# Performance work log

Hardware: AMD Instinct MI355X
Metric: run time of the kernel (lower is better)

## Reference

```python
import jax, jax.numpy as jnp
import numpy as np

N, IN_DIM, OUT_DIM = 8192, 256, 64
NEG_BIG = -9e15
LRELU_SLOPE = 0.01  # torch F.leaky_relu default


def setup_inputs() -> dict:
    key = jax.random.key(0)
    k1, k2, k3, k4 = jax.random.split(key, 4)
    inp = jax.random.normal(k1, (N, IN_DIM), dtype=jnp.float32)
    adj = jax.random.randint(k2, (N, N), 0, 2, dtype=jnp.int32)
    # xavier_uniform with gain=1.414
    limW = 1.414 * np.sqrt(6.0 / (IN_DIM + OUT_DIM))
    W = jax.random.uniform(k3, (IN_DIM, OUT_DIM), minval=-limW, maxval=limW, dtype=jnp.float32)
    lima = 1.414 * np.sqrt(6.0 / (2 * OUT_DIM + 1))
    a = jax.random.uniform(k4, (2 * OUT_DIM, 1), minval=-lima, maxval=lima, dtype=jnp.float32)
    return {"input": inp, "adj": adj, "W": W, "a": a}


def reference(input, adj, W, a):
    h = input @ W                      # [N, D]
    a1, a2 = a[:OUT_DIM, 0], a[OUT_DIM:, 0]
    # e[i,j] = leaky_relu(a1.h_i + a2.h_j) == the concat-based score, no NxNx2D tensor
    f1 = h @ a1                        # [N]
    f2 = h @ a2                        # [N]
    e = jax.nn.leaky_relu(f1[:, None] + f2[None, :], negative_slope=LRELU_SLOPE)  # [N, N]
    face_Rhand = e[1, 2]
    face_Lhand = e[1, 3]
    Rhand_Lhand = e[3, 2]
    attention = jnp.where(adj > 0, e, jnp.float32(NEG_BIG))
    alpha = jax.nn.softmax(attention, axis=1)
    h_prime = alpha @ h                # [N, D]
    return (h_prime, face_Rhand, face_Lhand, Rhand_Lhand)
```

## Files before the change

kernel.cpp:

```cpp
#include <hip/hip_runtime.h>
#include <hip/hip_bf16.h>

#define GN 8192
#define KD 256
#define OD 64
#define LOG2E 1.44269504f
#define ASTR 260
#define NCH 16

typedef __attribute__((ext_vector_type(8))) short bf16x8;
typedef __attribute__((ext_vector_type(4))) float f32x4;

__device__ __forceinline__ float fexp2(float x) {
#if __has_builtin(__builtin_amdgcn_exp2f)
  return __builtin_amdgcn_exp2f(x);
#else
  return exp2f(x);
#endif
}

__device__ __forceinline__ void async_cp16(const void* g, void* l) {
  __builtin_amdgcn_global_load_lds(
      (const __attribute__((address_space(1))) unsigned int*)g,
      (__attribute__((address_space(3))) unsigned int*)l, 16, 0, 0);
}

__global__ __launch_bounds__(256) void gat_k1(
    const float* __restrict__ input, const float* __restrict__ W,
    const float* __restrict__ a, __hip_bfloat16* __restrict__ hT,
    float* __restrict__ f1p, float* __restrict__ f2p, float* __restrict__ out)
{
  __shared__ float Wl[KD * OD];
  __shared__ float inT[KD * 33];
  __shared__ float red1[8][32];
  __shared__ float red2[8][32];
  __shared__ float s1row[32];
  __shared__ float s2row[32];

  const int tid = threadIdx.x;
  const int i0 = blockIdx.x * 32;

  for (int idx = tid; idx < KD * OD / 4; idx += 256)
    ((float4*)Wl)[idx] = ((const float4*)W)[idx];

#pragma unroll
  for (int it = 0; it < 8; ++it) {
    int idx = tid + it * 256;
    int r = idx >> 6, k4 = idx & 63;
    float4 v = *(const float4*)(input + (long)(i0 + r) * KD + k4 * 4);
    inT[(k4 * 4 + 0) * 33 + r] = v.x;
    inT[(k4 * 4 + 1) * 33 + r] = v.y;
    inT[(k4 * 4 + 2) * 33 + r] = v.z;
    inT[(k4 * 4 + 3) * 33 + r] = v.w;
  }
  __syncthreads();

  const int r = tid & 31;
  const int cg = tid >> 5;
  float acc[8];
#pragma unroll
  for (int c = 0; c < 8; ++c) acc[c] = 0.f;

#pragma unroll 4
  for (int k = 0; k < KD; ++k) {
    float inv = inT[k * 33 + r];
    float4 wa = *(const float4*)&Wl[k * 64 + cg * 8];
    float4 wb = *(const float4*)&Wl[k * 64 + cg * 8 + 4];
    acc[0] += inv * wa.x; acc[1] += inv * wa.y;
    acc[2] += inv * wa.z; acc[3] += inv * wa.w;
    acc[4] += inv * wb.x; acc[5] += inv * wb.y;
    acc[6] += inv * wb.z; acc[7] += inv * wb.w;
  }

#pragma unroll
  for (int c = 0; c < 8; ++c)
    hT[(long)(cg * 8 + c) * GN + i0 + r] = __float2bfloat16(acc[c]);

  float s1 = 0.f, s2 = 0.f;
#pragma unroll
  for (int c = 0; c < 8; ++c) {
    s1 += acc[c] * a[cg * 8 + c];
    s2 += acc[c] * a[OD + cg * 8 + c];
  }
  red1[cg][r] = s1; red2[cg][r] = s2;
  __syncthreads();
  if (tid < 32) {
    float f1 = 0.f, f2 = 0.f;
#pragma unroll
    for (int g = 0; g < 8; ++g) { f1 += red1[g][tid]; f2 += red2[g][tid]; }
    s1row[tid] = f1; s2row[tid] = f2;
    f1p[i0 + tid] = f1 * LOG2E;
    f2p[i0 + tid] = f2 * LOG2E;
  }
  __syncthreads();
  if (blockIdx.x == 0 && tid == 0) {
    float e12 = s1row[1] + s2row[2];
    float e13 = s1row[1] + s2row[3];
    float e32 = s1row[3] + s2row[2];
    out[(long)GN * OD + 0] = fmaxf(e12, 0.01f * e12);
    out[(long)GN * OD + 1] = fmaxf(e13, 0.01f * e13);
    out[(long)GN * OD + 2] = fmaxf(e32, 0.01f * e32);
  }
}

__global__ __launch_bounds__(256, 4) void gat_k2(
    const int* __restrict__ adj, const __hip_bfloat16* __restrict__ hT,
    const float* __restrict__ f1p, const float* __restrict__ f2p,
    float* __restrict__ pn, float* __restrict__ pd)
{
  __shared__ int smem[2 * 16 * ASTR];
  float* pb = (float*)smem;
  float* sb = pb + 4 * 16 * 68;

  const int tid = threadIdx.x;
  const int lane = tid & 63;
  const int wv = tid >> 6;
  const int tn = lane & 15;
  const int quad = lane >> 4;
  const int rg = blockIdx.x >> 1;
  const int js = blockIdx.x & 1;
  const int i0 = rg * 16;
  const int jbase = js * 4096;

  const float f1r = f1p[i0 + tn];
  const int jo0 = (2 * wv) * 32 + quad * 8;
  const int jo1 = jo0 + 32;
  const __hip_bfloat16* hbase = hT + (long)tn * GN + jbase;
  const float* fpb = f2p + jbase;

  const int srow = wv * 4;
  const int* g0 = adj + (long)(i0 + srow + 0) * GN + jbase + lane * 4;
  const int* g1 = adj + (long)(i0 + srow + 1) * GN + jbase + lane * 4;
  const int* g2 = adj + (long)(i0 + srow + 2) * GN + jbase + lane * 4;
  const int* g3 = adj + (long)(i0 + srow + 3) * GN + jbase + lane * 4;

  f32x4 acc[4];
#pragma unroll
  for (int nf = 0; nf < 4; ++nf) acc[nf] = (f32x4){0.f, 0.f, 0.f, 0.f};
  f32x4 accS = (f32x4){0.f, 0.f, 0.f, 0.f};

  bf16x8 ones;
  {
    short ov = (tn == 0) ? (short)0x3F80 : (short)0;
#pragma unroll
    for (int i = 0; i < 8; ++i) ones[i] = ov;
  }

  async_cp16(g0, &smem[(srow + 0) * ASTR]);
  async_cp16(g1, &smem[(srow + 1) * ASTR]);
  async_cp16(g2, &smem[(srow + 2) * ASTR]);
  async_cp16(g3, &smem[(srow + 3) * ASTR]);
  bf16x8 B0[4], B1[4];
#pragma unroll
  for (int nf = 0; nf < 4; ++nf) {
    B0[nf] = *(const bf16x8*)(hbase + (long)nf * (16 * GN) + jo0);
    B1[nf] = *(const bf16x8*)(hbase + (long)nf * (16 * GN) + jo1);
  }
  __syncthreads();

  for (int c = 0; c < NCH; ++c) {
    const int cur = (c & 1) * (16 * ASTR);
    const int nxt = ((c & 1) ^ 1) * (16 * ASTR);
    if (c + 1 < NCH) {
      async_cp16(g0 + (c + 1) * 256, &smem[nxt + (srow + 0) * ASTR]);
      async_cp16(g1 + (c + 1) * 256, &smem[nxt + (srow + 1) * ASTR]);
      async_cp16(g2 + (c + 1) * 256, &smem[nxt + (srow + 2) * ASTR]);
      async_cp16(g3 + (c + 1) * 256, &smem[nxt + (srow + 3) * ASTR]);
    }

    const float4 f20 = *(const float4*)(fpb + c * 256 + jo0);
    const float4 f21 = *(const float4*)(fpb + c * 256 + jo0 + 4);
    const float4 f22 = *(const float4*)(fpb + c * 256 + jo1);
    const float4 f23 = *(const float4*)(fpb + c * 256 + jo1 + 4);
    const int4 a0 = *(const int4*)&smem[cur + tn * ASTR + jo0];
    const int4 a1 = *(const int4*)&smem[cur + tn * ASTR + jo0 + 4];
    const int4 a2 = *(const int4*)&smem[cur + tn * ASTR + jo1];
    const int4 a3 = *(const int4*)&smem[cur + tn * ASTR + jo1 + 4];

    union { bf16x8 v; unsigned u[4]; } w0, w1;
    {
      float e0 = f1r + f20.x, e1 = f1r + f20.y, e2 = f1r + f20.z, e3 = f1r + f20.w;
      float e4 = f1r + f21.x, e5 = f1r + f21.y, e6 = f1r + f21.z, e7 = f1r + f21.w;
      float v0 = fexp2((a0.x > 0) ? fmaxf(e0, 0.01f * e0) : -256.f);
      float v1 = fexp2((a0.y > 0) ? fmaxf(e1, 0.01f * e1) : -256.f);
      float v2 = fexp2((a0.z > 0) ? fmaxf(e2, 0.01f * e2) : -256.f);
      float v3 = fexp2((a0.w > 0) ? fmaxf(e3, 0.01f * e3) : -256.f);
      float v4 = fexp2((a1.x > 0) ? fmaxf(e4, 0.01f * e4) : -256.f);
      float v5 = fexp2((a1.y > 0) ? fmaxf(e5, 0.01f * e5) : -256.f);
      float v6 = fexp2((a1.z > 0) ? fmaxf(e6, 0.01f * e6) : -256.f);
      float v7 = fexp2((a1.w > 0) ? fmaxf(e7, 0.01f * e7) : -256.f);
      w0.u[0] = __builtin_amdgcn_perm(__float_as_uint(v1), __float_as_uint(v0), 0x07060302u);
      w0.u[1] = __builtin_amdgcn_perm(__float_as_uint(v3), __float_as_uint(v2), 0x07060302u);
      w0.u[2] = __builtin_amdgcn_perm(__float_as_uint(v5), __float_as_uint(v4), 0x07060302u);
      w0.u[3] = __builtin_amdgcn_perm(__float_as_uint(v7), __float_as_uint(v6), 0x07060302u);
    }
    {
      float e0 = f1r + f22.x, e1 = f1r + f22.y, e2 = f1r + f22.z, e3 = f1r + f22.w;
      float e4 = f1r + f23.x, e5 = f1r + f23.y, e6 = f1r + f23.z, e7 = f1r + f23.w;
      float v0 = fexp2((a2.x > 0) ? fmaxf(e0, 0.01f * e0) : -256.f);
      float v1 = fexp2((a2.y > 0) ? fmaxf(e1, 0.01f * e1) : -256.f);
      float v2 = fexp2((a2.z > 0) ? fmaxf(e2, 0.01f * e2) : -256.f);
      float v3 = fexp2((a2.w > 0) ? fmaxf(e3, 0.01f * e3) : -256.f);
      float v4 = fexp2((a3.x > 0) ? fmaxf(e4, 0.01f * e4) : -256.f);
      float v5 = fexp2((a3.y > 0) ? fmaxf(e5, 0.01f * e5) : -256.f);
      float v6 = fexp2((a3.z > 0) ? fmaxf(e6, 0.01f * e6) : -256.f);
      float v7 = fexp2((a3.w > 0) ? fmaxf(e7, 0.01f * e7) : -256.f);
      w1.u[0] = __builtin_amdgcn_perm(__float_as_uint(v1), __float_as_uint(v0), 0x07060302u);
      w1.u[1] = __builtin_amdgcn_perm(__float_as_uint(v3), __float_as_uint(v2), 0x07060302u);
      w1.u[2] = __builtin_amdgcn_perm(__float_as_uint(v5), __float_as_uint(v4), 0x07060302u);
      w1.u[3] = __builtin_amdgcn_perm(__float_as_uint(v7), __float_as_uint(v6), 0x07060302u);
    }

#pragma unroll
    for (int nf = 0; nf < 4; ++nf)
      acc[nf] = __builtin_amdgcn_mfma_f32_16x16x32_bf16(w0.v, B0[nf], acc[nf], 0, 0, 0);
    accS = __builtin_amdgcn_mfma_f32_16x16x32_bf16(w0.v, ones, accS, 0, 0, 0);
#pragma unroll
    for (int nf = 0; nf < 4; ++nf)
      acc[nf] = __builtin_amdgcn_mfma_f32_16x16x32_bf16(w1.v, B1[nf], acc[nf], 0, 0, 0);
    accS = __builtin_amdgcn_mfma_f32_16x16x32_bf16(w1.v, ones, accS, 0, 0, 0);

    if (c + 1 < NCH) {
#pragma unroll
      for (int nf = 0; nf < 4; ++nf) {
        B0[nf] = *(const bf16x8*)(hbase + (long)nf * (16 * GN) + (c + 1) * 256 + jo0);
        B1[nf] = *(const bf16x8*)(hbase + (long)nf * (16 * GN) + (c + 1) * 256 + jo1);
      }
    }
    __syncthreads();
  }

#pragma unroll
  for (int nf = 0; nf < 4; ++nf)
#pragma unroll
    for (int rgi = 0; rgi < 4; ++rgi)
      pb[(wv * 16 + quad * 4 + rgi) * 68 + nf * 16 + tn] = acc[nf][rgi];
  if (tn == 0) {
#pragma unroll
    for (int rgi = 0; rgi < 4; ++rgi)
      sb[wv * 16 + quad * 4 + rgi] = accS[rgi];
  }
  __syncthreads();
  for (int t = tid; t < 16 * OD; t += 256) {
    int rr = t >> 6, cc = t & 63;
    float num = pb[(0 * 16 + rr) * 68 + cc] + pb[(1 * 16 + rr) * 68 + cc] +
                pb[(2 * 16 + rr) * 68 + cc] + pb[(3 * 16 + rr) * 68 + cc];
    pn[((long)js * GN + i0 + rr) * OD + cc] = num;
  }
  if (tid < 16) {
    float den = sb[0 * 16 + tid] + sb[1 * 16 + tid] + sb[2 * 16 + tid] + sb[3 * 16 + tid];
    pd[(long)js * GN + i0 + tid] = den;
  }
}

__global__ __launch_bounds__(256) void gat_k3(
    const float* __restrict__ pn, const float* __restrict__ pd,
    float* __restrict__ out)
{
  long t = (long)blockIdx.x * 256 + threadIdx.x;
  int i = (int)(t >> 6);
  float num = pn[t] + pn[(long)GN * OD + t];
  float den = pd[i] + pd[GN + i];
  out[t] = num / den;
}

extern "C" void kernel_launch(void* const* d_in, const int* in_sizes, int n_in,
                              void* d_out, int out_size, void* d_ws, size_t ws_size,
                              hipStream_t stream) {
  const float* input = (const float*)d_in[0];
  const int* adj     = (const int*)d_in[1];
  const float* W     = (const float*)d_in[2];
  const float* a     = (const float*)d_in[3];
  float* out = (float*)d_out;

  char* ws = (char*)d_ws;
  __hip_bfloat16* hT = (__hip_bfloat16*)ws;
  float* f1p = (float*)(ws + (size_t)OD * GN * 2);
  float* f2p = f1p + GN;
  float* pn  = f2p + GN;
  float* pd  = pn + (size_t)2 * GN * OD;

  gat_k1<<<256, 256, 0, stream>>>(input, W, a, hT, f1p, f2p, out);
  gat_k2<<<1024, 256, 0, stream>>>(adj, hT, f1p, f2p, pn, pd);
  gat_k3<<<GN * OD / 256, 256, 0, stream>>>(pn, pd, out);
}
```

Before: 400.8 us.

## Tile h layout per 32 rows, stage f2 in LDS, register-staged adj prefetch

```diff
diff --git a/kernel.cpp b/kernel.cpp
--- a/kernel.cpp
+++ b/kernel.cpp
@@ -19,15 +19,9 @@
 #endif
 }
 
-__device__ __forceinline__ void async_cp16(const void* g, void* l) {
-  __builtin_amdgcn_global_load_lds(
-      (const __attribute__((address_space(1))) unsigned int*)g,
-      (__attribute__((address_space(3))) unsigned int*)l, 16, 0, 0);
-}
-
 __global__ __launch_bounds__(256) void gat_k1(
     const float* __restrict__ input, const float* __restrict__ W,
-    const float* __restrict__ a, __hip_bfloat16* __restrict__ hT,
+    const float* __restrict__ a, __hip_bfloat16* __restrict__ hTt,
     float* __restrict__ f1p, float* __restrict__ f2p, float* __restrict__ out)
 {
   __shared__ float Wl[KD * OD];
@@ -74,7 +68,8 @@
 
 #pragma unroll
   for (int c = 0; c < 8; ++c)
-    hT[(long)(cg * 8 + c) * GN + i0 + r] = __float2bfloat16(acc[c]);
+    hTt[(long)blockIdx.x * (OD * 32) + (cg * 8 + c) * 32 + r] =
+        __float2bfloat16(acc[c]);
 
   float s1 = 0.f, s2 = 0.f;
 #pragma unroll
@@ -103,13 +98,14 @@
   }
 }
 
-__global__ __launch_bounds__(256, 4) void gat_k2(
-    const int* __restrict__ adj, const __hip_bfloat16* __restrict__ hT,
+__global__ __launch_bounds__(256, 3) void gat_k2(
+    const int* __restrict__ adj, const __hip_bfloat16* __restrict__ hTt,
     const float* __restrict__ f1p, const float* __restrict__ f2p,
     float* __restrict__ pn, float* __restrict__ pd)
 {
-  __shared__ int smem[2 * 16 * ASTR];
-  float* pb = (float*)smem;
+  __shared__ int abuf[2][16 * ASTR];
+  __shared__ float f2l[4096];
+  float* pb = (float*)abuf;
   float* sb = pb + 4 * 16 * 68;
 
   const int tid = threadIdx.x;
@@ -122,17 +118,18 @@
   const int i0 = rg * 16;
   const int jbase = js * 4096;
 
+  for (int i = tid; i < 4096 / 4; i += 256)
+    ((float4*)f2l)[i] = ((const float4*)(f2p + jbase))[i];
+
   const float f1r = f1p[i0 + tn];
-  const int jo0 = (2 * wv) * 32 + quad * 8;
+
+  const int sr = tid >> 4;
+  const int sc = (tid & 15) * 4;
+  const int* gsrc = adj + (long)(i0 + sr) * GN + jbase + sc;
+
+  const int jo0 = wv * 64 + quad * 8;
   const int jo1 = jo0 + 32;
-  const __hip_bfloat16* hbase = hT + (long)tn * GN + jbase;
-  const float* fpb = f2p + jbase;
-
-  const int srow = wv * 4;
-  const int* g0 = adj + (long)(i0 + srow + 0) * GN + jbase + lane * 4;
-  const int* g1 = adj + (long)(i0 + srow + 1) * GN + jbase + lane * 4;
-  const int* g2 = adj + (long)(i0 + srow + 2) * GN + jbase + lane * 4;
-  const int* g3 = adj + (long)(i0 + srow + 3) * GN + jbase + lane * 4;
+  const __hip_bfloat16* hsl = hTt + (long)(jbase / 32) * (OD * 32) + tn * 32 + quad * 8;
 
   f32x4 acc[4];
 #pragma unroll
@@ -146,36 +143,39 @@
     for (int i = 0; i < 8; ++i) ones[i] = ov;
   }
 
-  async_cp16(g0, &smem[(srow + 0) * ASTR]);
-  async_cp16(g1, &smem[(srow + 1) * ASTR]);
-  async_cp16(g2, &smem[(srow + 2) * ASTR]);
-  async_cp16(g3, &smem[(srow + 3) * ASTR]);
-  bf16x8 B0[4], B1[4];
-#pragma unroll
-  for (int nf = 0; nf < 4; ++nf) {
-    B0[nf] = *(const bf16x8*)(hbase + (long)nf * (16 * GN) + jo0);
-    B1[nf] = *(const bf16x8*)(hbase + (long)nf * (16 * GN) + jo1);
-  }
+  int4 st[4];
+#pragma unroll
+  for (int k = 0; k < 4; ++k) st[k] = *(const int4*)(gsrc + 64 * k);
+#pragma unroll
+  for (int k = 0; k < 4; ++k) *(int4*)&abuf[0][sr * ASTR + sc + 64 * k] = st[k];
   __syncthreads();
 
   for (int c = 0; c < NCH; ++c) {
-    const int cur = (c & 1) * (16 * ASTR);
-    const int nxt = ((c & 1) ^ 1) * (16 * ASTR);
+    const int cur = c & 1, nxt = cur ^ 1;
+
+    const __hip_bfloat16* h0 = hsl + (long)(c * 8 + 2 * wv) * (OD * 32);
+    const __hip_bfloat16* h1 = h0 + (OD * 32);
+    bf16x8 B0[4], B1[4];
+#pragma unroll
+    for (int nf = 0; nf < 4; ++nf) {
+      B0[nf] = *(const bf16x8*)(h0 + nf * (16 * 32));
+      B1[nf] = *(const bf16x8*)(h1 + nf * (16 * 32));
+    }
+
     if (c + 1 < NCH) {
-      async_cp16(g0 + (c + 1) * 256, &smem[nxt + (srow + 0) * ASTR]);
-      async_cp16(g1 + (c + 1) * 256, &smem[nxt + (srow + 1) * ASTR]);
-      async_cp16(g2 + (c + 1) * 256, &smem[nxt + (srow + 2) * ASTR]);
-      async_cp16(g3 + (c + 1) * 256, &smem[nxt + (srow + 3) * ASTR]);
-    }
-
-    const float4 f20 = *(const float4*)(fpb + c * 256 + jo0);
-    const float4 f21 = *(const float4*)(fpb + c * 256 + jo0 + 4);
-    const float4 f22 = *(const float4*)(fpb + c * 256 + jo1);
-    const float4 f23 = *(const float4*)(fpb + c * 256 + jo1 + 4);
-    const int4 a0 = *(const int4*)&smem[cur + tn * ASTR + jo0];
-    const int4 a1 = *(const int4*)&smem[cur + tn * ASTR + jo0 + 4];
-    const int4 a2 = *(const int4*)&smem[cur + tn * ASTR + jo1];
-    const int4 a3 = *(const int4*)&smem[cur + tn * ASTR + jo1 + 4];
+#pragma unroll
+      for (int k = 0; k < 4; ++k)
+        st[k] = *(const int4*)(gsrc + (c + 1) * 256 + 64 * k);
+    }
+
+    const int4 a0 = *(const int4*)&abuf[cur][tn * ASTR + jo0];
+    const int4 a1 = *(const int4*)&abuf[cur][tn * ASTR + jo0 + 4];
+    const int4 a2 = *(const int4*)&abuf[cur][tn * ASTR + jo1];
+    const int4 a3 = *(const int4*)&abuf[cur][tn * ASTR + jo1 + 4];
+    const float4 f20 = *(const float4*)&f2l[c * 256 + jo0];
+    const float4 f21 = *(const float4*)&f2l[c * 256 + jo0 + 4];
+    const float4 f22 = *(const float4*)&f2l[c * 256 + jo1];
+    const float4 f23 = *(const float4*)&f2l[c * 256 + jo1 + 4];
 
     union { bf16x8 v; unsigned u[4]; } w0, w1;
     {
@@ -222,10 +222,8 @@
 
     if (c + 1 < NCH) {
 #pragma unroll
-      for (int nf = 0; nf < 4; ++nf) {
-        B0[nf] = *(const bf16x8*)(hbase + (long)nf * (16 * GN) + (c + 1) * 256 + jo0);
-        B1[nf] = *(const bf16x8*)(hbase + (long)nf * (16 * GN) + (c + 1) * 256 + jo1);
-      }
+      for (int k = 0; k < 4; ++k)
+        *(int4*)&abuf[nxt][sr * ASTR + sc + 64 * k] = st[k];
     }
     __syncthreads();
   }
@@ -274,13 +272,13 @@
   float* out = (float*)d_out;
 
   char* ws = (char*)d_ws;
-  __hip_bfloat16* hT = (__hip_bfloat16*)ws;
+  __hip_bfloat16* hTt = (__hip_bfloat16*)ws;
   float* f1p = (float*)(ws + (size_t)OD * GN * 2);
   float* f2p = f1p + GN;
   float* pn  = f2p + GN;
   float* pd  = pn + (size_t)2 * GN * OD;
 
-  gat_k1<<<256, 256, 0, stream>>>(input, W, a, hT, f1p, f2p, out);
-  gat_k2<<<1024, 256, 0, stream>>>(adj, hT, f1p, f2p, pn, pd);
+  gat_k1<<<256, 256, 0, stream>>>(input, W, a, hTt, f1p, f2p, out);
+  gat_k2<<<1024, 256, 0, stream>>>(adj, hTt, f1p, f2p, pn, pd);
   gat_k3<<<GN * OD / 256, 256, 0, stream>>>(pn, pd, out);
 }
```

After: 388.7 us. 1.03x faster.
